# Performance work log

Measured on AMD Instinct MI355X. Metric: run time of the kernel, lower is better.

Reference implementation:

```python
import jax, jax.numpy as jnp
import numpy as np

NO = 16          # config['Max_Object']
NT = 8           # config['Max_Time']
FEAT = 512       # config['feat_dims']
VIS_IN = 2048
TGT = 24


def setup_inputs() -> dict:
    key = jax.random.key(0)
    ks = jax.random.split(key, 10)
    b = 16
    N = NT * 2 * NO  # 256
    s = lambda k, *sh: jax.random.normal(k, sh, dtype=jnp.float32) * 0.02
    return {
        "src": jax.random.normal(ks[0], (b, 1, 1, N, VIS_IN), dtype=jnp.float32),
        "tgt_rel": jax.random.randint(ks[1], (b * NT * NO * NO,), 0, TGT, dtype=jnp.int64),
        "w1": s(ks[2], VIS_IN, FEAT), "b1": jnp.zeros((FEAT,), jnp.float32),
        "w2": s(ks[3], FEAT, FEAT),   "b2": jnp.zeros((FEAT,), jnp.float32),
        "wf": s(ks[4], FEAT, FEAT),   "bf": jnp.zeros((FEAT,), jnp.float32),
        "wr": s(ks[5], 2 * FEAT, TGT), "br": jnp.zeros((TGT,), jnp.float32),
    }


def reference(src, tgt_rel, w1, b1, w2, b2, wf, bf, wr, br):
    b = src.shape[0]
    BT = b * NT
    # src[:, 0, 0, :, :] -> (b, N, D) -> (b*NT, 2*NO, D); take visual part [:2048]
    x = src[:, 0, 0, :, :].reshape(BT, 2 * NO, -1)[:, :, :VIS_IN]
    # fc_vis: MLP 2048 -> FEAT -> FEAT
    h = jnp.maximum(x @ w1 + b1, 0.0) @ w2 + b2          # (BT, 2NO, FEAT)
    node_feats = h @ wf + bf                             # fc_fusion
    # vectorized replacement of the NOxNO python double loop:
    # edge[:, i*NO + (j-NO), :] = cat(node[:, i], node[:, j])  for i<NO<=j
    subj = jnp.broadcast_to(node_feats[:, :NO, None, :], (BT, NO, NO, FEAT))
    obj = jnp.broadcast_to(node_feats[:, None, NO:, :], (BT, NO, NO, FEAT))
    edge_feats = jnp.concatenate([subj, obj], axis=-1).reshape(BT, NO * NO, 2 * FEAT)
    out = (edge_feats @ wr + br).reshape(-1, TGT)        # fc_rel
    tgt = tgt_rel.reshape(-1)
    w_cls = jnp.asarray([1.0] + [100.0] * (TGT - 1), dtype=out.dtype)
    logp = jax.nn.log_softmax(out, axis=-1)
    nll = -jnp.take_along_axis(logp, tgt[:, None], axis=1)[:, 0]
    ww = w_cls[tgt]
    loss = jnp.sum(ww * nll) / jnp.sum(ww)  # torch weighted cross_entropy (mean)
    return out, tgt, loss
```

## Files before the change

kernel.cpp:

```cpp
#include <hip/hip_runtime.h>
#include <cstddef>
#include <cstdint>

#define NOBJ   16
#define FEAT   512
#define VIS    2048
#define NTGT   24
#define MROWS  4096
#define EROWS  32768

typedef __attribute__((ext_vector_type(8))) short short8;
typedef __attribute__((ext_vector_type(4))) float f32x4;

__device__ __forceinline__ unsigned short f2bf(float f) {
    union { float f; unsigned int i; } v; v.f = f;
    const unsigned int x = v.i;
    return (unsigned short)((x + 0x7fffu + ((x >> 16) & 1u)) >> 16);
}
__device__ __forceinline__ short8 pack8(const float4 a, const float4 b) {
    short8 r;
    r[0] = (short)f2bf(a.x); r[1] = (short)f2bf(a.y);
    r[2] = (short)f2bf(a.z); r[3] = (short)f2bf(a.w);
    r[4] = (short)f2bf(b.x); r[5] = (short)f2bf(b.y);
    r[6] = (short)f2bf(b.z); r[7] = (short)f2bf(b.w);
    return r;
}

__global__ __launch_bounds__(256)
void wtrans(const float* __restrict__ w1, unsigned short* __restrict__ w1t) {
    __shared__ float tile[32][33];
    const int k0 = blockIdx.x * 32;
    const int n0 = blockIdx.y * 32;
    const int tx = threadIdx.x & 31, ty = threadIdx.x >> 5;
    #pragma unroll
    for (int r = 0; r < 32; r += 8)
        tile[ty + r][tx] = w1[(size_t)(k0 + ty + r) * FEAT + n0 + tx];
    __syncthreads();
    #pragma unroll
    for (int r = 0; r < 32; r += 8)
        w1t[(size_t)(n0 + ty + r) * VIS + k0 + tx] = f2bf(tile[tx][ty + r]);
}

__global__ __launch_bounds__(256)
void wchain1(const float* __restrict__ wf, const float* __restrict__ bfv,
             const float* __restrict__ wr, float* __restrict__ t1) {
    __shared__ float wrs[FEAT * NTGT];
    const int h = blockIdx.y;
    const float* wrh = wr + (size_t)h * FEAT * NTGT;
    for (int idx = threadIdx.y * 32 + threadIdx.x; idx < FEAT * NTGT; idx += 256)
        wrs[idx] = wrh[idx];
    __syncthreads();
    const int c    = threadIdx.x;
    const int krow = blockIdx.x * 8 + threadIdx.y;
    if (krow > 512) return;
    const float* rowp = (krow < 512) ? (wf + (size_t)krow * FEAT) : bfv;
    const int ce = (c < NTGT) ? c : NTGT - 1;
    float s = 0.f;
    #pragma unroll 8
    for (int j = 0; j < FEAT; ++j)
        s = fmaf(rowp[j], wrs[j * NTGT + ce], s);
    if (c < NTGT) t1[((size_t)h * 513 + krow) * 32 + c] = s;
}

__global__ __launch_bounds__(256)
void wchain2(const float* __restrict__ w2, const float* __restrict__ b2,
             const float* __restrict__ t1, unsigned short* __restrict__ wABt,
             float* __restrict__ biasAB) {
    __shared__ float t1s[FEAT * NTGT];
    const int h = blockIdx.y;
    for (int idx = threadIdx.y * 32 + threadIdx.x; idx < FEAT * NTGT; idx += 256) {
        const int row = idx / NTGT, col = idx - row * NTGT;
        t1s[idx] = t1[((size_t)h * 513 + row) * 32 + col];
    }
    __syncthreads();
    const int c = threadIdx.x;
    const int r = blockIdx.x * 8 + threadIdx.y;
    if (r > 512) return;
    const float* rowp = (r < 512) ? (w2 + (size_t)r * FEAT) : b2;
    const int ce = (c < NTGT) ? c : NTGT - 1;
    float s = 0.f;
    #pragma unroll 8
    for (int k = 0; k < FEAT; ++k)
        s = fmaf(rowp[k], t1s[k * NTGT + ce], s);
    if (c < NTGT) {
        const int q = h * NTGT + c;
        if (r < 512) wABt[(size_t)q * FEAT + r] = f2bf(s);
        else         biasAB[q] = s + t1[((size_t)h * 513 + 512) * 32 + c];
    }
}

__global__ __launch_bounds__(256)
void gemm1(const float* __restrict__ src, const unsigned short* __restrict__ w1t,
           const float* __restrict__ b1, unsigned short* __restrict__ h) {
    __shared__ __align__(16) unsigned short As[2][128 * 64];
    __shared__ __align__(16) unsigned short Bs[2][32 * 64];

    const int bid = blockIdx.x;
    const int xcd = bid & 7;
    const int k8  = bid >> 3;
    const int xb  = k8 & 15;
    const int yb  = (xcd << 2) | (k8 >> 4);
    const int m0 = yb * 128;
    const int n0 = xb * 32;

    const int tid  = threadIdx.x;
    const int lane = tid & 63;
    const int wid  = tid >> 6;

    f32x4  acc[2][2] = {};
    float4 areg[4][2];
    short8 breg;

    #pragma unroll
    for (int q = 0; q < 4; ++q) {
        const int s = q * 256 + tid, row = s >> 3, c = s & 7, cd = c ^ (row & 7);
        const float* gp = src + (size_t)(m0 + row) * VIS + (cd << 3);
        areg[q][0] = *reinterpret_cast<const float4*>(gp);
        areg[q][1] = *reinterpret_cast<const float4*>(gp + 4);
    }
    {
        const int n = tid >> 3, c = tid & 7, cd = c ^ (n & 7);
        breg = *reinterpret_cast<const short8*>(w1t + (size_t)(n0 + n) * VIS + (cd << 3));
    }
    #pragma unroll
    for (int q = 0; q < 4; ++q) {
        const int s = q * 256 + tid, row = s >> 3, c = s & 7;
        *reinterpret_cast<short8*>(&As[0][(row << 6) + (c << 3)]) = pack8(areg[q][0], areg[q][1]);
    }
    {
        const int n = tid >> 3, c = tid & 7;
        *reinterpret_cast<short8*>(&Bs[0][(n << 6) + (c << 3)]) = breg;
    }
    __syncthreads();

    int cur = 0;
    for (int t = 0; t < VIS / 64; ++t) {
        const int kn = (t + 1) * 64;
        if (t + 1 < VIS / 64) {
            #pragma unroll
            for (int q = 0; q < 4; ++q) {
                const int s = q * 256 + tid, row = s >> 3, c = s & 7, cd = c ^ (row & 7);
                const float* gp = src + (size_t)(m0 + row) * VIS + kn + (cd << 3);
                areg[q][0] = *reinterpret_cast<const float4*>(gp);
                areg[q][1] = *reinterpret_cast<const float4*>(gp + 4);
            }
            const int n = tid >> 3, c = tid & 7, cd = c ^ (n & 7);
            breg = *reinterpret_cast<const short8*>(w1t + (size_t)(n0 + n) * VIS + kn + (cd << 3));
        }
        #pragma unroll
        for (int k2 = 0; k2 < 2; ++k2) {
            short8 af[2], bfr[2];
            #pragma unroll
            for (int fr = 0; fr < 2; ++fr) {
                const int row = wid * 32 + fr * 16 + (lane & 15);
                const int cw  = ((k2 << 2) + (lane >> 4)) ^ (row & 7);
                af[fr] = *reinterpret_cast<const short8*>(&As[cur][(row << 6) + (cw << 3)]);
            }
            #pragma unroll
            for (int fc = 0; fc < 2; ++fc) {
                const int n  = fc * 16 + (lane & 15);
                const int cw = ((k2 << 2) + (lane >> 4)) ^ (n & 7);
                bfr[fc] = *reinterpret_cast<const short8*>(&Bs[cur][(n << 6) + (cw << 3)]);
            }
            #pragma unroll
            for (int fr = 0; fr < 2; ++fr)
                #pragma unroll
                for (int fc = 0; fc < 2; ++fc)
                    acc[fr][fc] = __builtin_amdgcn_mfma_f32_16x16x32_bf16(
                        af[fr], bfr[fc], acc[fr][fc], 0, 0, 0);
        }
        if (t + 1 < VIS / 64) {
            const int nxt = cur ^ 1;
            #pragma unroll
            for (int q = 0; q < 4; ++q) {
                const int s = q * 256 + tid, row = s >> 3, c = s & 7;
                *reinterpret_cast<short8*>(&As[nxt][(row << 6) + (c << 3)]) =
                    pack8(areg[q][0], areg[q][1]);
            }
            const int n = tid >> 3, c = tid & 7;
            *reinterpret_cast<short8*>(&Bs[nxt][(n << 6) + (c << 3)]) = breg;
        }
        __syncthreads();
        cur ^= 1;
    }

    #pragma unroll
    for (int fc = 0; fc < 2; ++fc) {
        const int n = n0 + fc * 16 + (lane & 15);
        const float bias = b1[n];
        #pragma unroll
        for (int fr = 0; fr < 2; ++fr) {
            const int mb = m0 + wid * 32 + fr * 16 + ((lane >> 4) << 2);
            #pragma unroll
            for (int r = 0; r < 4; ++r) {
                const float v = fmaxf(acc[fr][fc][r] + bias, 0.f);
                h[(size_t)(mb + r) * FEAT + n] = f2bf(v);
            }
        }
    }
}

__global__ __launch_bounds__(256)
void projG(const unsigned short* __restrict__ h, const unsigned short* __restrict__ wABt,
           const float* __restrict__ biasAB, float* __restrict__ P) {
    __shared__ __align__(16) unsigned short Bs[64 * 512];
    __shared__ __align__(16) unsigned short As[32 * 64];
    const int tid  = threadIdx.x;
    const int lane = tid & 63;
    const int wid  = tid >> 6;
    const int m0   = blockIdx.x * 32;

    #pragma unroll
    for (int q = 0; q < 16; ++q) {
        const int e = q * 256 + tid;
        const int n = e >> 6, cc = e & 63, cd = cc ^ (n & 7);
        *reinterpret_cast<short8*>(&Bs[(n << 9) + (cc << 3)]) =
            *reinterpret_cast<const short8*>(wABt + ((size_t)n << 9) + (cd << 3));
    }
    __syncthreads();

    f32x4 acc[2] = {};
    for (int t = 0; t < FEAT / 64; ++t) {
        const int kt = t * 64;
        {
            const int row = tid >> 3, c = tid & 7, cd = c ^ (row & 7);
            *reinterpret_cast<short8*>(&As[(row << 6) + (c << 3)]) =
                *reinterpret_cast<const short8*>(h + (size_t)(m0 + row) * FEAT + kt + (cd << 3));
        }
        __syncthreads();
        #pragma unroll
        for (int k2 = 0; k2 < 2; ++k2) {
            short8 af[2], bfr;
            #pragma unroll
            for (int fr = 0; fr < 2; ++fr) {
                const int row = fr * 16 + (lane & 15);
                const int cw  = ((k2 << 2) + (lane >> 4)) ^ (row & 7);
                af[fr] = *reinterpret_cast<const short8*>(&As[(row << 6) + (cw << 3)]);
            }
            {
                const int n     = wid * 16 + (lane & 15);
                const int chunk = t * 8 + k2 * 4 + (lane >> 4);
                const int cw    = chunk ^ (n & 7);
                bfr = *reinterpret_cast<const short8*>(&Bs[(n << 9) + (cw << 3)]);
            }
            #pragma unroll
            for (int fr = 0; fr < 2; ++fr)
                acc[fr] = __builtin_amdgcn_mfma_f32_16x16x32_bf16(af[fr], bfr, acc[fr], 0, 0, 0);
        }
        __syncthreads();
    }

    const int n = wid * 16 + (lane & 15);
    const float bias = biasAB[n];
    #pragma unroll
    for (int fr = 0; fr < 2; ++fr) {
        const int rb = fr * 16 + ((lane >> 4) << 2);
        #pragma unroll
        for (int r = 0; r < 4; ++r)
            P[(size_t)(m0 + rb + r) * 64 + n] = acc[fr][r] + bias;
    }
}

__global__ __launch_bounds__(256)
void out_loss_kernel(const float* __restrict__ P, const float* __restrict__ br,
                     const int* __restrict__ tgt, float* __restrict__ out,
                     float* __restrict__ out_tgt, float* __restrict__ partials) {
    __shared__ float sm[32][49];
    const int bt  = blockIdx.x;
    const int tid = threadIdx.x;
    for (int idx = tid; idx < 32 * 48; idx += 256) {
        const int row = idx / 48, col = idx - row * 48;
        sm[row][col] = P[(size_t)(bt * 32 + row) * 64 + col];
    }
    __syncthreads();

    const int r  = bt * 256 + tid;
    const int i  = tid >> 4, j = tid & 15;
    const int tg = tgt[r];

    float vals[NTGT];
    float mx = -1e30f, vtg = 0.f;
    #pragma unroll
    for (int t = 0; t < NTGT; ++t) {
        const float v = sm[i][t] + sm[16 + j][24 + t] + br[t];
        vals[t] = v;
        mx = fmaxf(mx, v);
        if (t == tg) vtg = v;
    }
    float se = 0.f;
    #pragma unroll
    for (int t = 0; t < NTGT; ++t) se += expf(vals[t] - mx);
    const float lse = mx + logf(se);

    float4* o4 = reinterpret_cast<float4*>(out + (size_t)r * NTGT);
    #pragma unroll
    for (int q = 0; q < 6; ++q)
        o4[q] = make_float4(vals[q * 4], vals[q * 4 + 1], vals[q * 4 + 2], vals[q * 4 + 3]);
    out_tgt[r] = (float)tg;

    const float wcl = (tg == 0) ? 1.f : 100.f;
    float p1 = wcl * (lse - vtg);
    float p2 = wcl;
    #pragma unroll
    for (int off = 32; off > 0; off >>= 1) {
        p1 += __shfl_down(p1, off);
        p2 += __shfl_down(p2, off);
    }
    __shared__ float s1[4], s2[4];
    const int lane = tid & 63, wv = tid >> 6;
    if (lane == 0) { s1[wv] = p1; s2[wv] = p2; }
    __syncthreads();
    if (tid == 0) {
        partials[bt]       = s1[0] + s1[1] + s1[2] + s1[3];
        partials[128 + bt] = s2[0] + s2[1] + s2[2] + s2[3];
    }
}

__global__ void final_loss(const float* __restrict__ partials, float* __restrict__ loss) {
    const int t = threadIdx.x;
    float a = partials[t] + partials[t + 64];
    float b = partials[128 + t] + partials[192 + t];
    #pragma unroll
    for (int off = 32; off > 0; off >>= 1) {
        a += __shfl_down(a, off);
        b += __shfl_down(b, off);
    }
    if (t == 0) loss[0] = a / b;
}

extern "C" void kernel_launch(void* const* d_in, const int* in_sizes, int n_in,
                              void* d_out, int out_size, void* d_ws, size_t ws_size,
                              hipStream_t stream) {
    const float* src = (const float*)d_in[0];
    const int*   tgt = (const int*)d_in[1];
    const float* w1  = (const float*)d_in[2];
    const float* b1  = (const float*)d_in[3];
    const float* w2  = (const float*)d_in[4];
    const float* b2  = (const float*)d_in[5];
    const float* wf  = (const float*)d_in[6];
    const float* bfv = (const float*)d_in[7];
    const float* wr  = (const float*)d_in[8];
    const float* br  = (const float*)d_in[9];

    float* ws = (float*)d_ws;
    unsigned short* w1t  = (unsigned short*)(ws);
    unsigned short* h    = (unsigned short*)(ws + 524288);
    float*          t1   = ws + 1572864;
    unsigned short* wABt = (unsigned short*)(ws + 1605696);
    float*          biasAB = ws + 1622080;
    float*          P    = ws + 1622144;
    float*          parts = ws + 1884288;

    float* out_logits = (float*)d_out;
    float* out_tgt    = out_logits + (size_t)EROWS * NTGT;
    float* out_lossp  = out_tgt + EROWS;

    wtrans<<<dim3(64, 16), 256, 0, stream>>>(w1, w1t);
    wchain1<<<dim3(65, 2), dim3(32, 8), 0, stream>>>(wf, bfv, wr, t1);
    wchain2<<<dim3(65, 2), dim3(32, 8), 0, stream>>>(w2, b2, t1, wABt, biasAB);
    gemm1<<<512, 256, 0, stream>>>(src, w1t, b1, h);
    projG<<<128, 256, 0, stream>>>(h, wABt, biasAB, P);
    out_loss_kernel<<<128, 256, 0, stream>>>(P, br, tgt, out_logits, out_tgt, parts);
    final_loss<<<1, 64, 0, stream>>>(parts, out_lossp);
}
```

Before: 163.7 us.

## Fuse projection GEMM into first GEMM epilogue and merge prep kernels

```diff
diff --git a/kernel.cpp b/kernel.cpp
--- a/kernel.cpp
+++ b/kernel.cpp
@@ -12,6 +12,9 @@
 typedef __attribute__((ext_vector_type(8))) short short8;
 typedef __attribute__((ext_vector_type(4))) float f32x4;
 
+__device__ __forceinline__ float bf2f(unsigned short u) {
+    union { unsigned int i; float f; } v; v.i = ((unsigned int)u) << 16; return v.f;
+}
 __device__ __forceinline__ unsigned short f2bf(float f) {
     union { float f; unsigned int i; } v; v.f = f;
     const unsigned int x = v.i;
@@ -27,61 +30,71 @@
 }
 
 __global__ __launch_bounds__(256)
-void wtrans(const float* __restrict__ w1, unsigned short* __restrict__ w1t) {
-    __shared__ float tile[32][33];
-    const int k0 = blockIdx.x * 32;
-    const int n0 = blockIdx.y * 32;
-    const int tx = threadIdx.x & 31, ty = threadIdx.x >> 5;
-    #pragma unroll
-    for (int r = 0; r < 32; r += 8)
-        tile[ty + r][tx] = w1[(size_t)(k0 + ty + r) * FEAT + n0 + tx];
-    __syncthreads();
-    #pragma unroll
-    for (int r = 0; r < 32; r += 8)
-        w1t[(size_t)(n0 + ty + r) * VIS + k0 + tx] = f2bf(tile[tx][ty + r]);
+void prep1(const float* __restrict__ w1, unsigned short* __restrict__ w1t,
+           const float* __restrict__ wf, const float* __restrict__ bfv,
+           const float* __restrict__ wr, float* __restrict__ t1) {
+    __shared__ float shbuf[FEAT * NTGT];
+    const int b   = blockIdx.x;
+    const int tid = threadIdx.x;
+    if (b < 1024) {
+        float (*tile)[33] = (float(*)[33])shbuf;
+        const int k0 = (b & 63) * 32;
+        const int n0 = (b >> 6) * 32;
+        const int tx = tid & 31, ty = tid >> 5;
+        #pragma unroll
+        for (int r = 0; r < 32; r += 8)
+            tile[ty + r][tx] = w1[(size_t)(k0 + ty + r) * FEAT + n0 + tx];
+        __syncthreads();
+        #pragma unroll
+        for (int r = 0; r < 32; r += 8)
+            w1t[(size_t)(n0 + ty + r) * VIS + k0 + tx] = f2bf(tile[tx][ty + r]);
+    } else {
+        const int bb = b - 1024;
+        const int h  = bb & 1;
+        const float* wrh = wr + (size_t)h * FEAT * NTGT;
+        for (int idx = tid; idx < FEAT * NTGT; idx += 256)
+            shbuf[idx] = wrh[idx];
+        __syncthreads();
+        const int c    = tid & 31;
+        const int krow = (bb >> 1) * 8 + (tid >> 5);
+        if (krow > 512) return;
+        const float* rowp = (krow < 512) ? (wf + (size_t)krow * FEAT) : bfv;
+        const int ce = (c < NTGT) ? c : NTGT - 1;
+        float s = 0.f;
+        #pragma unroll 8
+        for (int j = 0; j < FEAT; ++j)
+            s = fmaf(rowp[j], shbuf[j * NTGT + ce], s);
+        if (c < NTGT) t1[((size_t)h * 513 + krow) * 32 + c] = s;
+    }
 }
 
 __global__ __launch_bounds__(256)
-void wchain1(const float* __restrict__ wf, const float* __restrict__ bfv,
-             const float* __restrict__ wr, float* __restrict__ t1) {
-    __shared__ float wrs[FEAT * NTGT];
-    const int h = blockIdx.y;
-    const float* wrh = wr + (size_t)h * FEAT * NTGT;
-    for (int idx = threadIdx.y * 32 + threadIdx.x; idx < FEAT * NTGT; idx += 256)
-        wrs[idx] = wrh[idx];
-    __syncthreads();
-    const int c    = threadIdx.x;
-    const int krow = blockIdx.x * 8 + threadIdx.y;
-    if (krow > 512) return;
-    const float* rowp = (krow < 512) ? (wf + (size_t)krow * FEAT) : bfv;
-    const int ce = (c < NTGT) ? c : NTGT - 1;
-    float s = 0.f;
-    #pragma unroll 8
-    for (int j = 0; j < FEAT; ++j)
-        s = fmaf(rowp[j], wrs[j * NTGT + ce], s);
-    if (c < NTGT) t1[((size_t)h * 513 + krow) * 32 + c] = s;
-}
-
-__global__ __launch_bounds__(256)
-void wchain2(const float* __restrict__ w2, const float* __restrict__ b2,
-             const float* __restrict__ t1, unsigned short* __restrict__ wABt,
-             float* __restrict__ biasAB) {
-    __shared__ float t1s[FEAT * NTGT];
-    const int h = blockIdx.y;
-    for (int idx = threadIdx.y * 32 + threadIdx.x; idx < FEAT * NTGT; idx += 256) {
+void prep2(const float* __restrict__ w2, const float* __restrict__ b2,
+           const float* __restrict__ t1, unsigned short* __restrict__ wABt,
+           float* __restrict__ biasAB, float* __restrict__ P) {
+    __shared__ float shbuf[FEAT * NTGT];
+    const int b   = blockIdx.x;
+    const int tid = threadIdx.x;
+    if (b < 1024) {
+        P[(size_t)b * 256 + tid] = 0.f;
+        return;
+    }
+    const int bb = b - 1024;
+    const int h  = bb & 1;
+    for (int idx = tid; idx < FEAT * NTGT; idx += 256) {
         const int row = idx / NTGT, col = idx - row * NTGT;
-        t1s[idx] = t1[((size_t)h * 513 + row) * 32 + col];
-    }
-    __syncthreads();
-    const int c = threadIdx.x;
-    const int r = blockIdx.x * 8 + threadIdx.y;
+        shbuf[idx] = t1[((size_t)h * 513 + row) * 32 + col];
+    }
+    __syncthreads();
+    const int c = tid & 31;
+    const int r = (bb >> 1) * 8 + (tid >> 5);
     if (r > 512) return;
     const float* rowp = (r < 512) ? (w2 + (size_t)r * FEAT) : b2;
     const int ce = (c < NTGT) ? c : NTGT - 1;
     float s = 0.f;
     #pragma unroll 8
     for (int k = 0; k < FEAT; ++k)
-        s = fmaf(rowp[k], t1s[k * NTGT + ce], s);
+        s = fmaf(rowp[k], shbuf[k * NTGT + ce], s);
     if (c < NTGT) {
         const int q = h * NTGT + c;
         if (r < 512) wABt[(size_t)q * FEAT + r] = f2bf(s);
@@ -90,29 +103,31 @@
 }
 
 __global__ __launch_bounds__(256)
-void gemm1(const float* __restrict__ src, const unsigned short* __restrict__ w1t,
-           const float* __restrict__ b1, unsigned short* __restrict__ h) {
-    __shared__ __align__(16) unsigned short As[2][128 * 64];
+void gemm1f(const float* __restrict__ src, const unsigned short* __restrict__ w1t,
+            const float* __restrict__ b1, const unsigned short* __restrict__ wABt,
+            float* __restrict__ P) {
+    __shared__ __align__(16) unsigned short As[2][64 * 64];
     __shared__ __align__(16) unsigned short Bs[2][32 * 64];
 
     const int bid = blockIdx.x;
     const int xcd = bid & 7;
     const int k8  = bid >> 3;
     const int xb  = k8 & 15;
-    const int yb  = (xcd << 2) | (k8 >> 4);
-    const int m0 = yb * 128;
+    const int yb  = (xcd << 3) | (k8 >> 4);
+    const int m0 = yb * 64;
     const int n0 = xb * 32;
 
     const int tid  = threadIdx.x;
     const int lane = tid & 63;
     const int wid  = tid >> 6;
-
-    f32x4  acc[2][2] = {};
-    float4 areg[4][2];
+    const int wr = wid >> 1, wc = wid & 1;
+
+    f32x4  acc[2] = {};
+    float4 areg[2][2];
     short8 breg;
 
     #pragma unroll
-    for (int q = 0; q < 4; ++q) {
+    for (int q = 0; q < 2; ++q) {
         const int s = q * 256 + tid, row = s >> 3, c = s & 7, cd = c ^ (row & 7);
         const float* gp = src + (size_t)(m0 + row) * VIS + (cd << 3);
         areg[q][0] = *reinterpret_cast<const float4*>(gp);
@@ -123,7 +138,7 @@
         breg = *reinterpret_cast<const short8*>(w1t + (size_t)(n0 + n) * VIS + (cd << 3));
     }
     #pragma unroll
-    for (int q = 0; q < 4; ++q) {
+    for (int q = 0; q < 2; ++q) {
         const int s = q * 256 + tid, row = s >> 3, c = s & 7;
         *reinterpret_cast<short8*>(&As[0][(row << 6) + (c << 3)]) = pack8(areg[q][0], areg[q][1]);
     }
@@ -138,7 +153,7 @@
         const int kn = (t + 1) * 64;
         if (t + 1 < VIS / 64) {
             #pragma unroll
-            for (int q = 0; q < 4; ++q) {
+            for (int q = 0; q < 2; ++q) {
                 const int s = q * 256 + tid, row = s >> 3, c = s & 7, cd = c ^ (row & 7);
                 const float* gp = src + (size_t)(m0 + row) * VIS + kn + (cd << 3);
                 areg[q][0] = *reinterpret_cast<const float4*>(gp);
@@ -149,30 +164,26 @@
         }
         #pragma unroll
         for (int k2 = 0; k2 < 2; ++k2) {
-            short8 af[2], bfr[2];
+            short8 af[2], bfr;
             #pragma unroll
             for (int fr = 0; fr < 2; ++fr) {
-                const int row = wid * 32 + fr * 16 + (lane & 15);
+                const int row = wr * 32 + fr * 16 + (lane & 15);
                 const int cw  = ((k2 << 2) + (lane >> 4)) ^ (row & 7);
                 af[fr] = *reinterpret_cast<const short8*>(&As[cur][(row << 6) + (cw << 3)]);
             }
-            #pragma unroll
-            for (int fc = 0; fc < 2; ++fc) {
-                const int n  = fc * 16 + (lane & 15);
+            {
+                const int n  = wc * 16 + (lane & 15);
                 const int cw = ((k2 << 2) + (lane >> 4)) ^ (n & 7);
-                bfr[fc] = *reinterpret_cast<const short8*>(&Bs[cur][(n << 6) + (cw << 3)]);
+                bfr = *reinterpret_cast<const short8*>(&Bs[cur][(n << 6) + (cw << 3)]);
             }
             #pragma unroll
             for (int fr = 0; fr < 2; ++fr)
-                #pragma unroll
-                for (int fc = 0; fc < 2; ++fc)
-                    acc[fr][fc] = __builtin_amdgcn_mfma_f32_16x16x32_bf16(
-                        af[fr], bfr[fc], acc[fr][fc], 0, 0, 0);
+                acc[fr] = __builtin_amdgcn_mfma_f32_16x16x32_bf16(af[fr], bfr, acc[fr], 0, 0, 0);
         }
         if (t + 1 < VIS / 64) {
             const int nxt = cur ^ 1;
             #pragma unroll
-            for (int q = 0; q < 4; ++q) {
+            for (int q = 0; q < 2; ++q) {
                 const int s = q * 256 + tid, row = s >> 3, c = s & 7;
                 *reinterpret_cast<short8*>(&As[nxt][(row << 6) + (c << 3)]) =
                     pack8(areg[q][0], areg[q][1]);
@@ -184,87 +195,50 @@
         cur ^= 1;
     }
 
-    #pragma unroll
-    for (int fc = 0; fc < 2; ++fc) {
-        const int n = n0 + fc * 16 + (lane & 15);
-        const float bias = b1[n];
+    short8 bq[3];
+    #pragma unroll
+    for (int t3 = 0; t3 < 3; ++t3)
+        bq[t3] = *reinterpret_cast<const short8*>(
+            wABt + (size_t)(t3 * 16 + (lane & 15)) * FEAT + n0 + ((lane >> 4) << 3));
+
+    unsigned short* Ht = &As[0][0];
+    {
+        const int nl   = wc * 16 + (lane & 15);
+        const float bias = b1[n0 + nl];
         #pragma unroll
         for (int fr = 0; fr < 2; ++fr) {
-            const int mb = m0 + wid * 32 + fr * 16 + ((lane >> 4) << 2);
+            const int ml = wr * 32 + fr * 16 + ((lane >> 4) << 2);
             #pragma unroll
             for (int r = 0; r < 4; ++r) {
-                const float v = fmaxf(acc[fr][fc][r] + bias, 0.f);
-                h[(size_t)(mb + r) * FEAT + n] = f2bf(v);
+                const float v = fmaxf(acc[fr][r] + bias, 0.f);
+                Ht[(ml + r) * 40 + nl] = f2bf(v);
             }
         }
     }
-}
-
-__global__ __launch_bounds__(256)
-void projG(const unsigned short* __restrict__ h, const unsigned short* __restrict__ wABt,
-           const float* __restrict__ biasAB, float* __restrict__ P) {
-    __shared__ __align__(16) unsigned short Bs[64 * 512];
-    __shared__ __align__(16) unsigned short As[32 * 64];
-    const int tid  = threadIdx.x;
-    const int lane = tid & 63;
-    const int wid  = tid >> 6;
-    const int m0   = blockIdx.x * 32;
-
-    #pragma unroll
-    for (int q = 0; q < 16; ++q) {
-        const int e = q * 256 + tid;
-        const int n = e >> 6, cc = e & 63, cd = cc ^ (n & 7);
-        *reinterpret_cast<short8*>(&Bs[(n << 9) + (cc << 3)]) =
-            *reinterpret_cast<const short8*>(wABt + ((size_t)n << 9) + (cd << 3));
-    }
-    __syncthreads();
-
-    f32x4 acc[2] = {};
-    for (int t = 0; t < FEAT / 64; ++t) {
-        const int kt = t * 64;
-        {
-            const int row = tid >> 3, c = tid & 7, cd = c ^ (row & 7);
-            *reinterpret_cast<short8*>(&As[(row << 6) + (c << 3)]) =
-                *reinterpret_cast<const short8*>(h + (size_t)(m0 + row) * FEAT + kt + (cd << 3));
-        }
-        __syncthreads();
-        #pragma unroll
-        for (int k2 = 0; k2 < 2; ++k2) {
-            short8 af[2], bfr;
-            #pragma unroll
-            for (int fr = 0; fr < 2; ++fr) {
-                const int row = fr * 16 + (lane & 15);
-                const int cw  = ((k2 << 2) + (lane >> 4)) ^ (row & 7);
-                af[fr] = *reinterpret_cast<const short8*>(&As[(row << 6) + (cw << 3)]);
-            }
-            {
-                const int n     = wid * 16 + (lane & 15);
-                const int chunk = t * 8 + k2 * 4 + (lane >> 4);
-                const int cw    = chunk ^ (n & 7);
-                bfr = *reinterpret_cast<const short8*>(&Bs[(n << 9) + (cw << 3)]);
-            }
-            #pragma unroll
-            for (int fr = 0; fr < 2; ++fr)
-                acc[fr] = __builtin_amdgcn_mfma_f32_16x16x32_bf16(af[fr], bfr, acc[fr], 0, 0, 0);
-        }
-        __syncthreads();
-    }
-
-    const int n = wid * 16 + (lane & 15);
-    const float bias = biasAB[n];
-    #pragma unroll
-    for (int fr = 0; fr < 2; ++fr) {
-        const int rb = fr * 16 + ((lane >> 4) << 2);
+    __syncthreads();
+
+    short8 aep;
+    {
+        const int m = wid * 16 + (lane & 15);
+        aep = *reinterpret_cast<const short8*>(&Ht[m * 40 + ((lane >> 4) << 3)]);
+    }
+    const f32x4 pz = {0.f, 0.f, 0.f, 0.f};
+    #pragma unroll
+    for (int t3 = 0; t3 < 3; ++t3) {
+        f32x4 pp = __builtin_amdgcn_mfma_f32_16x16x32_bf16(aep, bq[t3], pz, 0, 0, 0);
+        const int q  = t3 * 16 + (lane & 15);
+        const int mb = m0 + wid * 16 + ((lane >> 4) << 2);
         #pragma unroll
         for (int r = 0; r < 4; ++r)
-            P[(size_t)(m0 + rb + r) * 64 + n] = acc[fr][r] + bias;
+            atomicAdd(&P[(size_t)(mb + r) * 64 + q], pp[r]);
     }
 }
 
 __global__ __launch_bounds__(256)
 void out_loss_kernel(const float* __restrict__ P, const float* __restrict__ br,
-                     const int* __restrict__ tgt, float* __restrict__ out,
-                     float* __restrict__ out_tgt, float* __restrict__ partials) {
+                     const float* __restrict__ biasAB, const int* __restrict__ tgt,
+                     float* __restrict__ out, float* __restrict__ out_tgt,
+                     float* __restrict__ partials) {
     __shared__ float sm[32][49];
     const int bt  = blockIdx.x;
     const int tid = threadIdx.x;
@@ -282,7 +256,8 @@
     float mx = -1e30f, vtg = 0.f;
     #pragma unroll
     for (int t = 0; t < NTGT; ++t) {
-        const float v = sm[i][t] + sm[16 + j][24 + t] + br[t];
+        const float cv = br[t] + biasAB[t] + biasAB[24 + t];
+        const float v  = sm[i][t] + sm[16 + j][24 + t] + cv;
         vals[t] = v;
         mx = fmaxf(mx, v);
         if (t == tg) vtg = v;
@@ -344,22 +319,20 @@
 
     float* ws = (float*)d_ws;
     unsigned short* w1t  = (unsigned short*)(ws);
-    unsigned short* h    = (unsigned short*)(ws + 524288);
-    float*          t1   = ws + 1572864;
-    unsigned short* wABt = (unsigned short*)(ws + 1605696);
-    float*          biasAB = ws + 1622080;
-    float*          P    = ws + 1622144;
-    float*          parts = ws + 1884288;
+    float*          t1   = ws + 524288;
+    unsigned short* wABt = (unsigned short*)(ws + 557056);
+    float*          biasAB = ws + 569344;
+    float*          P    = ws + 569408;
+    float*          parts = ws + 831552;
 
     float* out_logits = (float*)d_out;
     float* out_tgt    = out_logits + (size_t)EROWS * NTGT;
     float* out_lossp  = out_tgt + EROWS;
 
-    wtrans<<<dim3(64, 16), 256, 0, stream>>>(w1, w1t);
-    wchain1<<<dim3(65, 2), dim3(32, 8), 0, stream>>>(wf, bfv, wr, t1);
-    wchain2<<<dim3(65, 2), dim3(32, 8), 0, stream>>>(w2, b2, t1, wABt, biasAB);
-    gemm1<<<512, 256, 0, stream>>>(src, w1t, b1, h);
-    projG<<<128, 256, 0, stream>>>(h, wABt, biasAB, P);
-    out_loss_kernel<<<128, 256, 0, stream>>>(P, br, tgt, out_logits, out_tgt, parts);
+    prep1<<<1154, 256, 0, stream>>>(w1, w1t, wf, bfv, wr, t1);
+    prep2<<<1154, 256, 0, stream>>>(w2, b2, t1, wABt, biasAB, P);
+    gemm1f<<<1024, 256, 0, stream>>>(src, w1t, b1, wABt, P);
+    out_loss_kernel<<<128, 256, 0, stream>>>(P, br, biasAB, tgt,
+                                             out_logits, out_tgt, parts);
     final_loss<<<1, 64, 0, stream>>>(parts, out_lossp);
 }
```

Result: faster. 156.5 us (-4.4%).
